# Performance work log

Measured on AMD Instinct MI355X. Metric: run time of the kernel, lower is better.

The kernel has to match this reference:

```python
import jax, jax.numpy as jnp
import numpy as np

B, L, V = 32, 1024, 64
PL = 16                 # patch_len == stride
PH = L // PL            # p_his = 64
PRED = 512
PF = PRED // PL         # p_future = 32
D = 128                 # embed_dim
H = 256                 # hidden_dim
K = 1024                # n_clusters
TOPK = 5
TEMP = 1.0
EPS = 1e-5


def _layernorm(x, w, b):
    mu = jnp.mean(x, axis=-1, keepdims=True)
    var = jnp.mean((x - mu) ** 2, axis=-1, keepdims=True)
    return (x - mu) * jax.lax.rsqrt(var + 1e-5) * w + b


def setup_inputs() -> dict:
    key = jax.random.key(0)
    ks = jax.random.split(key, 12)
    s = 0.02
    return {
        "x": jax.random.normal(ks[0], (B, L, V), jnp.float32),
        "centroids": jax.random.normal(ks[1], (K, D), jnp.float32),
        "enc_w": jax.random.normal(ks[2], (PL, D), jnp.float32) * s,
        "enc_b": jnp.zeros((D,), jnp.float32),
        "ln_w": jnp.ones((D,), jnp.float32),
        "ln_b": jnp.zeros((D,), jnp.float32),
        "fc1_w": jax.random.normal(ks[3], (PH, H), jnp.float32) * s,
        "fc1_b": jnp.zeros((H,), jnp.float32),
        "fcm_w": jax.random.normal(ks[4], (H, 2 * H), jnp.float32) * s,
        "fcm_b": jnp.zeros((2 * H,), jnp.float32),
        "fc2_w": jax.random.normal(ks[5], (2 * H, PF), jnp.float32) * s,
        "fc2_b": jnp.zeros((PF,), jnp.float32),
        "fuse_w": jax.random.normal(ks[6], (D, D), jnp.float32) * s,
        "fuse_b": jnp.zeros((D,), jnp.float32),
        "fln_w": jnp.ones((D,), jnp.float32),
        "fln_b": jnp.zeros((D,), jnp.float32),
        "dec_w": jax.random.normal(ks[7], (D, PL), jnp.float32) * s,
        "dec_b": jnp.zeros((PL,), jnp.float32),
    }


def reference(x, centroids, enc_w, enc_b, ln_w, ln_b, fc1_w, fc1_b, fcm_w, fcm_b,
              fc2_w, fc2_b, fuse_w, fuse_b, fln_w, fln_b, dec_w, dec_b):
    # RevIN 'norm': per-(B,V) instance normalization over L
    mean = jnp.mean(x, axis=1, keepdims=True)               # [B,1,V]
    std = jnp.sqrt(jnp.var(x, axis=1, keepdims=True) + EPS)  # [B,1,V]
    xn = (x - mean) / std
    # patchify: [B,V,L] -> [B,V,PH,PL] (stride == patch_len)
    patches = jnp.transpose(xn, (0, 2, 1)).reshape(B, V, PH, PL)
    # vqvae.encode: per-patch linear patch_len -> D
    z_his = patches @ enc_w + enc_b                          # [B,V,PH,D]
    # TemporalMLPProjector: mix along the patch axis per channel dim
    h = _layernorm(z_his, ln_w, ln_b)
    h = jnp.transpose(h, (0, 1, 3, 2)).reshape(-1, PH)       # [B*V*D, PH]
    h = jax.nn.relu(h @ fc1_w + fc1_b)
    h = jax.nn.relu(h @ fcm_w + fcm_b)
    h = h @ fc2_w + fc2_b                                    # [B*V*D, PF]
    z_p = jnp.transpose(h.reshape(B, V, D, PF), (0, 1, 3, 2))  # [B,V,PF,D]
    # soft VQ: cdist^2 + top-k nearest + softmax-weighted codebook gather
    z_flat = z_p.reshape(-1, D)                              # [N,D], N=B*V*PF
    z2 = jnp.sum(z_flat ** 2, axis=-1, keepdims=True)        # [N,1]
    c2 = jnp.sum(centroids ** 2, axis=-1)                    # [K]
    zc = z_flat @ centroids.T                                # [N,K] GEMM
    dist = z2 + c2[None, :] - 2.0 * zc                       # [N,K]
    logits = (-dist / TEMP).reshape(B, V, PF, K)
    neg_topk, topk_idx = jax.lax.top_k(-dist, TOPK)          # smallest dists
    weights = jax.nn.softmax(neg_topk / TEMP, axis=-1)       # [N,TOPK]
    topk_c = centroids[topk_idx]                             # [N,TOPK,D] gather
    z_code = jnp.einsum('nk,nkd->nd', weights, topk_c).reshape(B, V, PF, D)
    # ResidualFusion: z_code + ReLU(Linear(z_p)), then LayerNorm
    z_fused = _layernorm(z_code + jax.nn.relu(z_p @ fuse_w + fuse_b), fln_w, fln_b)
    # vqvae.decode: per-patch linear D -> patch_len, then unpatchify
    rec_patches = z_fused @ dec_w + dec_b                    # [B,V,PF,PL]
    recon = jnp.transpose(rec_patches.reshape(B, V, PRED), (0, 2, 1))  # [B,PRED,V]
    outputs = recon * std + mean                              # RevIN 'denorm'
    return outputs, logits
```

## Files before the change

### kernel.cpp

```cpp
#include <hip/hip_runtime.h>
#include <float.h>
#include <math.h>


typedef __attribute__((ext_vector_type(8))) short bf16x8;
typedef __attribute__((ext_vector_type(4))) float f32x4;

__device__ __forceinline__ unsigned short f2bf(float f) {
  unsigned int u = __float_as_uint(f);
  u += 0x7FFFu + ((u >> 16) & 1u);
  return (unsigned short)(u >> 16);
}

__global__ __launch_bounds__(1024)
void k_stats(const float* __restrict__ x, float* __restrict__ stats) {
  __shared__ float s1[16][64];
  __shared__ float s2[16][64];
  const int v = threadIdx.x, seg = threadIdx.y, b = blockIdx.x;
  float a = 0.f, aa = 0.f;
  const float* xp = x + (b * 1024 + seg * 64) * 64 + v;
  for (int i = 0; i < 64; ++i) { const float t = xp[i * 64]; a += t; aa += t * t; }
  s1[seg][v] = a; s2[seg][v] = aa;
  __syncthreads();
  if (seg == 0) {
    float S = 0.f, SS = 0.f;
    for (int j = 0; j < 16; ++j) { S += s1[j][v]; SS += s2[j][v]; }
    const float mu  = S * (1.f / 1024.f);
    const float var = SS * (1.f / 1024.f) - mu * mu;
    const float sd  = sqrtf(var + 1e-5f);
    stats[b * 64 + v]        = mu;
    stats[2048 + b * 64 + v] = 1.f / sd;
    stats[4096 + b * 64 + v] = sd;
  }
}

__global__ __launch_bounds__(256)
void k_c2(const float* __restrict__ centroids, float* __restrict__ c2) {
  const int k = blockIdx.x * 256 + threadIdx.x;
  const float* cp = centroids + k * 128;
  float s = 0.f;
  for (int d = 0; d < 128; d += 4) {
    const float4 c = *(const float4*)(cp + d);
    s += c.x * c.x + c.y * c.y + c.z * c.z + c.w * c.w;
  }
  c2[k] = s;
}

__global__ __launch_bounds__(256)
void k_pack(const float* __restrict__ fc1_w, const float* __restrict__ fcm_w,
            const float* __restrict__ fc2_w,
            unsigned short* __restrict__ pk1, unsigned short* __restrict__ pk2,
            unsigned short* __restrict__ pk3) {
  const int idx = blockIdx.x * 256 + threadIdx.x;
  const int l  = idx & 63;
  const int kb = (l >> 4) * 8, nb = l & 15;
  unsigned short t[8];
  if (idx < 2048) {
    const int nt = idx >> 7, ks = (idx >> 6) & 1;
#pragma unroll
    for (int j = 0; j < 8; ++j)
      t[j] = f2bf(fc1_w[(ks * 32 + kb + j) * 256 + nt * 16 + nb]);
#pragma unroll
    for (int j = 0; j < 8; ++j) pk1[idx * 8 + j] = t[j];
  } else if (idx < 18432) {
    const int i2 = idx - 2048;
    const int nt = i2 >> 9, ks = (i2 >> 6) & 7;
#pragma unroll
    for (int j = 0; j < 8; ++j)
      t[j] = f2bf(fcm_w[(ks * 32 + kb + j) * 512 + nt * 16 + nb]);
#pragma unroll
    for (int j = 0; j < 8; ++j) pk2[i2 * 8 + j] = t[j];
  } else {
    const int i3 = idx - 18432;
    const int nt = i3 >> 10, ks = (i3 >> 6) & 15;
#pragma unroll
    for (int j = 0; j < 8; ++j)
      t[j] = f2bf(fc2_w[(ks * 32 + kb + j) * 32 + nt * 16 + nb]);
#pragma unroll
    for (int j = 0; j < 8; ++j) pk3[i3 * 8 + j] = t[j];
  }
}

__global__ __launch_bounds__(256)
void k_pack2(const float* __restrict__ centroids, const float* __restrict__ fuse_w,
             unsigned short* __restrict__ pkc, unsigned short* __restrict__ pkf) {
  const int idx = blockIdx.x * 256 + threadIdx.x;
  const int l  = idx & 63;
  const int kb = (l >> 4) * 8, nb = l & 15;
  unsigned short t[8];
  if (idx < 16384) {
    const int nt = idx >> 8;
#pragma unroll
    for (int j = 0; j < 8; ++j)
      t[j] = f2bf(centroids[(nt * 16 + nb) * 128 + ((idx >> 6) & 3) * 32 + kb + j]);
#pragma unroll
    for (int j = 0; j < 8; ++j) pkc[idx * 8 + j] = t[j];
  } else {
    const int i2 = idx - 16384;
    const int nt = i2 >> 8, ks = (i2 >> 6) & 3;
#pragma unroll
    for (int j = 0; j < 8; ++j)
      t[j] = f2bf(fuse_w[(ks * 32 + kb + j) * 128 + nt * 16 + nb]);
#pragma unroll
    for (int j = 0; j < 8; ++j) pkf[i2 * 8 + j] = t[j];
  }
}

__global__ __launch_bounds__(256, 2)
void k_mlp(const float* __restrict__ x,
           const float* __restrict__ enc_w, const float* __restrict__ enc_b,
           const float* __restrict__ ln_w,  const float* __restrict__ ln_b,
           const float* __restrict__ fc1_b, const float* __restrict__ fcm_b,
           const float* __restrict__ fc2_b,
           const unsigned short* __restrict__ pk1,
           const unsigned short* __restrict__ pk2,
           const unsigned short* __restrict__ pk3,
           const float* __restrict__ stats, float* __restrict__ z_p) {
  __shared__ __align__(16) char smem[65536];
  unsigned short* sh0 = (unsigned short*)smem;
  unsigned short* sh1 = (unsigned short*)(smem + 16384);
  unsigned short* sh2 = (unsigned short*)(smem + 49152);
  float* sxn = (float*)(smem + 16384);
  float* red = (float*)(smem + 20480);
  float* sew = (float*)(smem + 49152);

  const int tid  = threadIdx.x;
  const int lane = tid & 63, wv = tid >> 6;
  const int l15  = lane & 15, l16 = lane >> 4;
  const int bv   = blockIdx.x, b = bv >> 6, v = bv & 63;

  {
    const float mn = stats[bv], rs = stats[2048 + bv];
    const float* xb = x + b * 65536 + v;
    for (int i = tid; i < 1024; i += 256) sxn[i] = (xb[i * 64] - mn) * rs;
    for (int i = tid; i < 2048; i += 256) sew[i] = enc_w[i];
    __syncthreads();
    const int p = tid >> 2, qd = tid & 3;
    float xr[16];
#pragma unroll
    for (int t = 0; t < 16; ++t) xr[t] = sxn[p * 16 + t];
    float zv[32];
    float s1 = 0.f, s2 = 0.f;
#pragma unroll
    for (int dl = 0; dl < 32; ++dl) {
      const int d = qd * 32 + dl;
      float z = enc_b[d];
#pragma unroll
      for (int t = 0; t < 16; ++t) z += xr[t] * sew[t * 128 + d];
      zv[dl] = z; s1 += z; s2 += z * z;
    }
    red[p * 4 + qd] = s1; red[256 + p * 4 + qd] = s2;
    __syncthreads();
    const float S1 = red[p * 4] + red[p * 4 + 1] + red[p * 4 + 2] + red[p * 4 + 3];
    const float S2 = red[256 + p * 4] + red[256 + p * 4 + 1] +
                     red[256 + p * 4 + 2] + red[256 + p * 4 + 3];
    const float mu  = S1 * (1.f / 128.f);
    const float rsd = rsqrtf(S2 * (1.f / 128.f) - mu * mu + 1e-5f);
#pragma unroll
    for (int dl = 0; dl < 32; ++dl) {
      const int d = qd * 32 + dl;
      const float zn = (zv[dl] - mu) * rsd * ln_w[d] + ln_b[d];
      sh0[(d * 64 + p) ^ ((d & 7) << 3)] = f2bf(zn);
    }
  }
  __syncthreads();

  for (int hf = 0; hf < 2; ++hf) {
    {
      bf16x8 bf1[4][2];
#pragma unroll
      for (int nt = 0; nt < 4; ++nt) {
        const int ntg = wv * 4 + nt;
#pragma unroll
        for (int ks = 0; ks < 2; ++ks)
          bf1[nt][ks] = *(const bf16x8*)(pk1 + (((ntg * 2 + ks) * 64 + lane) << 3));
      }
      const int swa = (l15 & 7) << 3;
      bf16x8 am[4][2];
#pragma unroll
      for (int m = 0; m < 4; ++m) {
        const int row = hf * 64 + m * 16 + l15;
#pragma unroll
        for (int ks = 0; ks < 2; ++ks)
          am[m][ks] = *(const bf16x8*)(sh0 + ((row * 64 + ks * 32 + l16 * 8) ^ swa));
      }
      f32x4 acc1[4][4];
#pragma unroll
      for (int nt = 0; nt < 4; ++nt)
#pragma unroll
        for (int m = 0; m < 4; ++m) {
          f32x4 a; a[0] = 0.f; a[1] = 0.f; a[2] = 0.f; a[3] = 0.f;
          a = __builtin_amdgcn_mfma_f32_16x16x32_bf16(am[m][0], bf1[nt][0], a, 0, 0, 0);
          a = __builtin_amdgcn_mfma_f32_16x16x32_bf16(am[m][1], bf1[nt][1], a, 0, 0, 0);
          acc1[nt][m] = a;
        }
#pragma unroll
      for (int nt = 0; nt < 4; ++nt) {
        const int n = (wv * 4 + nt) * 16 + l15;
        const float bb = fc1_b[n];
#pragma unroll
        for (int m = 0; m < 4; ++m)
#pragma unroll
          for (int j = 0; j < 4; ++j) {
            const int r = m * 16 + l16 * 4 + j;
            const float vv = acc1[nt][m][j] + bb;
            sh1[(r * 256 + n) ^ ((r & 7) << 3)] = f2bf(vv > 0.f ? vv : 0.f);
          }
      }
    }
    __syncthreads();

    f32x4 accz[2];
#pragma unroll
    for (int nt = 0; nt < 2; ++nt) {
      const float bz = fc2_b[nt * 16 + l15];
      accz[nt][0] = bz; accz[nt][1] = bz; accz[nt][2] = bz; accz[nt][3] = bz;
    }

    for (int it = 0; it < 4; ++it) {
      bf16x8 bf2[2][8];
#pragma unroll
      for (int nt = 0; nt < 2; ++nt) {
        const int ntg = it * 8 + wv * 2 + nt;
#pragma unroll
        for (int ks = 0; ks < 8; ++ks)
          bf2[nt][ks] = *(const bf16x8*)(pk2 + (((ntg * 8 + ks) * 64 + lane) << 3));
      }
      f32x4 acc2[2][4];
#pragma unroll
      for (int nt = 0; nt < 2; ++nt)
#pragma unroll
        for (int m = 0; m < 4; ++m) {
          acc2[nt][m][0] = 0.f; acc2[nt][m][1] = 0.f;
          acc2[nt][m][2] = 0.f; acc2[nt][m][3] = 0.f;
        }
#pragma unroll
      for (int ks = 0; ks < 8; ++ks) {
        bf16x8 a2[4];
#pragma unroll
        for (int m = 0; m < 4; ++m) {
          const int row = m * 16 + l15;
          a2[m] = *(const bf16x8*)(sh1 +
                    ((row * 256 + ks * 32 + l16 * 8) ^ ((row & 7) << 3)));
        }
#pragma unroll
        for (int nt = 0; nt < 2; ++nt)
#pragma unroll
          for (int m = 0; m < 4; ++m)
            acc2[nt][m] = __builtin_amdgcn_mfma_f32_16x16x32_bf16(
                a2[m], bf2[nt][ks], acc2[nt][m], 0, 0, 0);
      }
#pragma unroll
      for (int nt = 0; nt < 2; ++nt) {
        const float bb = fcm_b[(it * 8 + wv * 2 + nt) * 16 + l15];
        const int c = (wv * 2 + nt) * 16 + l15;
#pragma unroll
        for (int m = 0; m < 4; ++m)
#pragma unroll
          for (int j = 0; j < 4; ++j) {
            const int r = m * 16 + l16 * 4 + j;
            const float vv = acc2[nt][m][j] + bb;
            sh2[(r * 128 + c) ^ ((r & 7) << 3)] = f2bf(vv > 0.f ? vv : 0.f);
          }
      }
      __syncthreads();
      {
        const int row = wv * 16 + l15;
        const int sw  = (row & 7) << 3;
        bf16x8 b3[2][4];
#pragma unroll
        for (int nt = 0; nt < 2; ++nt)
#pragma unroll
          for (int ks = 0; ks < 4; ++ks)
            b3[nt][ks] = *(const bf16x8*)(pk3 +
                           (((nt * 16 + it * 4 + ks) * 64 + lane) << 3));
#pragma unroll
        for (int ks = 0; ks < 4; ++ks) {
          const bf16x8 a3 = *(const bf16x8*)(sh2 +
                              ((row * 128 + ks * 32 + l16 * 8) ^ sw));
#pragma unroll
          for (int nt = 0; nt < 2; ++nt)
            accz[nt] = __builtin_amdgcn_mfma_f32_16x16x32_bf16(
                a3, b3[nt][ks], accz[nt], 0, 0, 0);
        }
      }
      __syncthreads();
    }

    {
      const int d0 = hf * 64 + wv * 16 + l16 * 4;
#pragma unroll
      for (int nt = 0; nt < 2; ++nt) {
        const int f = nt * 16 + l15;
        *(float4*)(z_p + (bv * 32 + f) * 128 + d0) =
            make_float4(accz[nt][0], accz[nt][1], accz[nt][2], accz[nt][3]);
      }
    }
  }
}

__global__ __launch_bounds__(256)
void k_vq(const float* __restrict__ z_p, const float* __restrict__ centroids,
          const float* __restrict__ c2g,
          const unsigned short* __restrict__ pkc,
          const unsigned short* __restrict__ pkf,
          const float* __restrict__ fuse_b,
          const float* __restrict__ fln_w,  const float* __restrict__ fln_b,
          const float* __restrict__ dec_w,  const float* __restrict__ dec_b,
          const float* __restrict__ stats,
          float* __restrict__ outputs, float* __restrict__ logits) {
  __shared__ __align__(16) char smem[23680];
  float* sdist = (float*)smem;
  float* zc    = (float*)smem;
  unsigned int* cand = (unsigned int*)(smem + 16896);
  float* z2s    = (float*)(smem + 22016);
  float* wrow   = (float*)(smem + 22144);
  int*   irow   = (int*)  (smem + 22784);
  float* lnstat = (float*)(smem + 23424);

  const int tid  = threadIdx.x;
  const int lane = tid & 63, wv = tid >> 6;
  const int l15  = lane & 15, l16 = lane >> 4;
  const int bv   = blockIdx.x, b = bv >> 6, v = bv & 63;

  bf16x8 za[2][4];
#pragma unroll
  for (int m = 0; m < 2; ++m)
#pragma unroll
    for (int ks = 0; ks < 4; ++ks) {
      const float* zp = z_p + (bv * 32 + m * 16 + l15) * 128 + ks * 32 + l16 * 8;
      const float4 u0 = *(const float4*)zp;
      const float4 u1 = *(const float4*)(zp + 4);
      bf16x8 t;
      t[0] = (short)f2bf(u0.x); t[1] = (short)f2bf(u0.y);
      t[2] = (short)f2bf(u0.z); t[3] = (short)f2bf(u0.w);
      t[4] = (short)f2bf(u1.x); t[5] = (short)f2bf(u1.y);
      t[6] = (short)f2bf(u1.z); t[7] = (short)f2bf(u1.w);
      za[m][ks] = t;
    }

  if (tid < 32) {
    const float* zp = z_p + (bv * 32 + tid) * 128;
    float s = 0.f;
    for (int d = 0; d < 128; d += 4) {
      const float4 u = *(const float4*)(zp + d);
      s += u.x * u.x + u.y * u.y + u.z * u.z + u.w * u.w;
    }
    z2s[tid] = s;
  }
  __syncthreads();

  float z2r[2][4];
#pragma unroll
  for (int m = 0; m < 2; ++m)
#pragma unroll
    for (int j = 0; j < 4; ++j) z2r[m][j] = z2s[m * 16 + l16 * 4 + j];

  unsigned int d5[5];
#pragma unroll
  for (int s = 0; s < 5; ++s) d5[s] = 0xFFFFFFFFu;

  const int row8 = tid >> 3, strip = tid & 7;

  for (int cc = 0; cc < 8; ++cc) {
    bf16x8 bfc[2][4];
#pragma unroll
    for (int nt = 0; nt < 2; ++nt) {
      const int ntg = cc * 8 + wv * 2 + nt;
#pragma unroll
      for (int ks = 0; ks < 4; ++ks)
        bfc[nt][ks] = *(const bf16x8*)(pkc + (((ntg * 4 + ks) * 64 + lane) << 3));
    }
    f32x4 acc[2][2];
#pragma unroll
    for (int nt = 0; nt < 2; ++nt)
#pragma unroll
      for (int m = 0; m < 2; ++m) {
        f32x4 a; a[0] = 0.f; a[1] = 0.f; a[2] = 0.f; a[3] = 0.f;
#pragma unroll
        for (int ks = 0; ks < 4; ++ks)
          a = __builtin_amdgcn_mfma_f32_16x16x32_bf16(za[m][ks], bfc[nt][ks], a, 0, 0, 0);
        acc[nt][m] = a;
      }
    if (cc) __syncthreads();
    {
      const float c2a = c2g[cc * 128 + (wv * 2) * 16 + l15];
      const float c2b = c2g[cc * 128 + (wv * 2 + 1) * 16 + l15];
#pragma unroll
      for (int nt = 0; nt < 2; ++nt) {
        const int colc = (wv * 2 + nt) * 16 + l15;
        const float cc2 = nt ? c2b : c2a;
#pragma unroll
        for (int m = 0; m < 2; ++m)
#pragma unroll
          for (int j = 0; j < 4; ++j) {
            const int r = m * 16 + l16 * 4 + j;
            sdist[r * 132 + colc] = z2r[m][j] + cc2 - 2.f * acc[nt][m][j];
          }
      }
    }
    __syncthreads();
#pragma unroll
    for (int i = 0; i < 4; ++i) {
      const int row = i * 8 + wv * 2 + (lane >> 5);
      const int c4  = (lane & 31) * 4;
      const float4 dv = *(const float4*)(sdist + row * 132 + c4);
      *(float4*)(logits + (bv * 32 + row) * 1024 + cc * 128 + c4) =
          make_float4(-dv.x, -dv.y, -dv.z, -dv.w);
    }
    for (int c = 0; c < 16; ++c) {
      const int col = strip + 8 * c;
      const float dvv = sdist[row8 * 132 + col];
      const unsigned int key =
          (__float_as_uint(dvv) & 0xFFFFFC00u) | (unsigned)(cc * 128 + col);
      if (key < d5[4]) {
        d5[4] = key;
        unsigned int t;
        if (d5[4] < d5[3]) { t = d5[3]; d5[3] = d5[4]; d5[4] = t; }
        if (d5[3] < d5[2]) { t = d5[2]; d5[2] = d5[3]; d5[3] = t; }
        if (d5[2] < d5[1]) { t = d5[1]; d5[1] = d5[2]; d5[2] = t; }
        if (d5[1] < d5[0]) { t = d5[0]; d5[0] = d5[1]; d5[1] = t; }
      }
    }
  }

#pragma unroll
  for (int s = 0; s < 5; ++s) cand[row8 * 40 + strip * 5 + s] = d5[s];
  __syncthreads();
  if (tid < 32) {
    unsigned int bk[5];
    for (int s = 0; s < 5; ++s) {
      unsigned int best = 0xFFFFFFFFu; int bpos = 0;
      for (int c = 0; c < 40; ++c) {
        const unsigned int u = cand[tid * 40 + c];
        if (u < best) { best = u; bpos = c; }
      }
      bk[s] = best; cand[tid * 40 + bpos] = 0xFFFFFFFFu;
    }
    float df[5];
#pragma unroll
    for (int j = 0; j < 5; ++j) df[j] = __uint_as_float(bk[j] & 0xFFFFFC00u);
    float e[5]; float sum = 0.f;
#pragma unroll
    for (int j = 0; j < 5; ++j) { e[j] = expf(df[0] - df[j]); sum += e[j]; }
    const float inv = 1.f / sum;
#pragma unroll
    for (int j = 0; j < 5; ++j) {
      wrow[tid * 5 + j] = e[j] * inv;
      irow[tid * 5 + j] = (int)(bk[j] & 1023u);
    }
  }
  __syncthreads();

  {
    const int r = tid >> 3, d0 = (tid & 7) * 16;
    float acc[16];
#pragma unroll
    for (int dd = 0; dd < 16; ++dd) acc[dd] = 0.f;
    for (int j = 0; j < 5; ++j) {
      const float w = wrow[r * 5 + j];
      const int   k = irow[r * 5 + j];
      const float* cp = centroids + k * 128 + d0;
#pragma unroll
      for (int dd = 0; dd < 16; dd += 4) {
        const float4 cv = *(const float4*)(cp + dd);
        acc[dd]   += w * cv.x; acc[dd+1] += w * cv.y;
        acc[dd+2] += w * cv.z; acc[dd+3] += w * cv.w;
      }
    }
#pragma unroll
    for (int dd = 0; dd < 16; dd += 4)
      *(float4*)(zc + r * 132 + d0 + dd) =
          make_float4(acc[dd], acc[dd+1], acc[dd+2], acc[dd+3]);
  }

  f32x4 fac[2][2];
  {
    bf16x8 bff[2][4];
#pragma unroll
    for (int nt = 0; nt < 2; ++nt) {
      const int ntg = wv * 2 + nt;
#pragma unroll
      for (int ks = 0; ks < 4; ++ks)
        bff[nt][ks] = *(const bf16x8*)(pkf + (((ntg * 4 + ks) * 64 + lane) << 3));
    }
#pragma unroll
    for (int nt = 0; nt < 2; ++nt)
#pragma unroll
      for (int m = 0; m < 2; ++m) {
        f32x4 a; a[0] = 0.f; a[1] = 0.f; a[2] = 0.f; a[3] = 0.f;
#pragma unroll
        for (int ks = 0; ks < 4; ++ks)
          a = __builtin_amdgcn_mfma_f32_16x16x32_bf16(za[m][ks], bff[nt][ks], a, 0, 0, 0);
        fac[nt][m] = a;
      }
  }
  __syncthreads();
#pragma unroll
  for (int nt = 0; nt < 2; ++nt) {
    const int colc = (wv * 2 + nt) * 16 + l15;
    const float fbv = fuse_b[colc];
#pragma unroll
    for (int m = 0; m < 2; ++m)
#pragma unroll
      for (int j = 0; j < 4; ++j) {
        const int r = m * 16 + l16 * 4 + j;
        zc[r * 132 + colc] += fmaxf(fac[nt][m][j] + fbv, 0.f);
      }
  }
  __syncthreads();

  if (tid < 32) {
    float s = 0.f, ss = 0.f;
    for (int d = 0; d < 128; ++d) { const float t = zc[tid * 132 + d]; s += t; ss += t * t; }
    const float mu  = s * (1.f / 128.f);
    const float var = ss * (1.f / 128.f) - mu * mu;
    lnstat[tid * 2]     = mu;
    lnstat[tid * 2 + 1] = rsqrtf(var + 1e-5f);
  }
  __syncthreads();

  {
    const int r = tid >> 3, tt = (tid & 7) * 2;
    const float mu = lnstat[r * 2], rsd = lnstat[r * 2 + 1];
    float o0 = dec_b[tt], o1 = dec_b[tt + 1];
    for (int d = 0; d < 128; ++d) {
      const float zf = (zc[r * 132 + d] - mu) * rsd * fln_w[d] + fln_b[d];
      o0 += zf * dec_w[d * 16 + tt];
      o1 += zf * dec_w[d * 16 + tt + 1];
    }
    const float sd = stats[4096 + bv], mn = stats[bv];
    outputs[(b * 512 + r * 16 + tt) * 64 + v]     = o0 * sd + mn;
    outputs[(b * 512 + r * 16 + tt + 1) * 64 + v] = o1 * sd + mn;
  }
}

extern "C" void kernel_launch(void* const* d_in, const int* in_sizes, int n_in,
                              void* d_out, int out_size, void* d_ws, size_t ws_size,
                              hipStream_t stream) {
  const float* x      = (const float*)d_in[0];
  const float* cent   = (const float*)d_in[1];
  const float* enc_w  = (const float*)d_in[2];
  const float* enc_b  = (const float*)d_in[3];
  const float* ln_w   = (const float*)d_in[4];
  const float* ln_b   = (const float*)d_in[5];
  const float* fc1_w  = (const float*)d_in[6];
  const float* fc1_b  = (const float*)d_in[7];
  const float* fcm_w  = (const float*)d_in[8];
  const float* fcm_b  = (const float*)d_in[9];
  const float* fc2_w  = (const float*)d_in[10];
  const float* fc2_b  = (const float*)d_in[11];
  const float* fuse_w = (const float*)d_in[12];
  const float* fuse_b = (const float*)d_in[13];
  const float* fln_w  = (const float*)d_in[14];
  const float* fln_b  = (const float*)d_in[15];
  const float* dec_w  = (const float*)d_in[16];
  const float* dec_b  = (const float*)d_in[17];

  float* ws    = (float*)d_ws;
  float* stats = ws;
  float* c2    = ws + 6144;
  float* z_p   = ws + 8192;
  unsigned short* pku = (unsigned short*)(ws + 8192 + 65536 * 128);
  unsigned short* pk1 = pku;
  unsigned short* pk2 = pku + 16384;
  unsigned short* pk3 = pku + 147456;
  unsigned short* pkc = pku + 163840;
  unsigned short* pkf = pku + 294912;

  float* outputs = (float*)d_out;
  float* logits  = (float*)d_out + 32 * 512 * 64;

  k_stats<<<dim3(32), dim3(64, 16), 0, stream>>>(x, stats);
  k_c2<<<dim3(4), dim3(256), 0, stream>>>(cent, c2);
  k_pack<<<dim3(80), dim3(256), 0, stream>>>(fc1_w, fcm_w, fc2_w, pk1, pk2, pk3);
  k_pack2<<<dim3(72), dim3(256), 0, stream>>>(cent, fuse_w, pkc, pkf);
  k_mlp<<<dim3(2048), dim3(256), 0, stream>>>(x, enc_w, enc_b, ln_w, ln_b,
      fc1_b, fcm_b, fc2_b, pk1, pk2, pk3, stats, z_p);
  k_vq<<<dim3(2048), dim3(256), 0, stream>>>(z_p, cent, c2, pkc, pkf, fuse_b,
      fln_w, fln_b, dec_w, dec_b, stats, outputs, logits);
}
```

Baseline: 600.4 us.

## Split fc2 reduction across waves by K-slice and drop per-iteration barriers

Each wave now multiplies only its own slice of the fc2 reduction dimension, using the sh2 columns it wrote itself, over all four row tiles. This removes the two __syncthreads per fcm/fc2 iteration. The partial sums from the four waves go to shared memory and are reduced, biased and stored to z_p in a final pass. The cost is more accumulator registers, an extra shared-memory staging and reduction step, and a smaller swizzle on sh2 writes that may bring back bank conflicts.

Result: slower. 637.3 us (+6.2%).

```diff
diff --git a/kernel.cpp b/kernel.cpp
--- a/kernel.cpp
+++ b/kernel.cpp
@@ -210,12 +210,14 @@
     }
     __syncthreads();
 
-    f32x4 accz[2];
-#pragma unroll
-    for (int nt = 0; nt < 2; ++nt) {
-      const float bz = fc2_b[nt * 16 + l15];
-      accz[nt][0] = bz; accz[nt][1] = bz; accz[nt][2] = bz; accz[nt][3] = bz;
-    }
+    f32x4 accz[2][4];
+#pragma unroll
+    for (int nt = 0; nt < 2; ++nt)
+#pragma unroll
+      for (int m = 0; m < 4; ++m) {
+        accz[nt][m][0] = 0.f; accz[nt][m][1] = 0.f;
+        accz[nt][m][2] = 0.f; accz[nt][m][3] = 0.f;
+      }
 
     for (int it = 0; it < 4; ++it) {
       bf16x8 bf2[2][8];
@@ -260,42 +262,57 @@
           for (int j = 0; j < 4; ++j) {
             const int r = m * 16 + l16 * 4 + j;
             const float vv = acc2[nt][m][j] + bb;
-            sh2[(r * 128 + c) ^ ((r & 7) << 3)] = f2bf(vv > 0.f ? vv : 0.f);
+            sh2[(r * 128 + c) ^ ((r & 3) << 3)] = f2bf(vv > 0.f ? vv : 0.f);
           }
       }
-      __syncthreads();
       {
-        const int row = wv * 16 + l15;
-        const int sw  = (row & 7) << 3;
-        bf16x8 b3[2][4];
+        bf16x8 b3[2];
 #pragma unroll
         for (int nt = 0; nt < 2; ++nt)
-#pragma unroll
-          for (int ks = 0; ks < 4; ++ks)
-            b3[nt][ks] = *(const bf16x8*)(pk3 +
-                           (((nt * 16 + it * 4 + ks) * 64 + lane) << 3));
-#pragma unroll
-        for (int ks = 0; ks < 4; ++ks) {
+          b3[nt] = *(const bf16x8*)(pk3 +
+                     (((nt * 16 + it * 4 + wv) * 64 + lane) << 3));
+#pragma unroll
+        for (int mt = 0; mt < 4; ++mt) {
+          const int row = mt * 16 + l15;
           const bf16x8 a3 = *(const bf16x8*)(sh2 +
-                              ((row * 128 + ks * 32 + l16 * 8) ^ sw));
+                              ((row * 128 + wv * 32 + l16 * 8) ^ ((row & 3) << 3)));
 #pragma unroll
           for (int nt = 0; nt < 2; ++nt)
-            accz[nt] = __builtin_amdgcn_mfma_f32_16x16x32_bf16(
-                a3, b3[nt][ks], accz[nt], 0, 0, 0);
+            accz[nt][mt] = __builtin_amdgcn_mfma_f32_16x16x32_bf16(
+                a3, b3[nt], accz[nt][mt], 0, 0, 0);
         }
       }
-      __syncthreads();
-    }
+    }
+    __syncthreads();
 
     {
-      const int d0 = hf * 64 + wv * 16 + l16 * 4;
+      float* part = (float*)(smem + 16384) + wv * 3072;
 #pragma unroll
       for (int nt = 0; nt < 2; ++nt) {
         const int f = nt * 16 + l15;
-        *(float4*)(z_p + (bv * 32 + f) * 128 + d0) =
-            make_float4(accz[nt][0], accz[nt][1], accz[nt][2], accz[nt][3]);
-      }
-    }
+#pragma unroll
+        for (int m = 0; m < 4; ++m)
+#pragma unroll
+          for (int j = 0; j < 4; ++j)
+            part[(m * 16 + l16 * 4 + j) * 33 + f] = accz[nt][m][j];
+      }
+    }
+    __syncthreads();
+    {
+      const float* P = (float*)(smem + 16384);
+      const int f = tid >> 3, r0 = (tid & 7) * 8;
+      const float bz = fc2_b[f];
+      float o[8];
+#pragma unroll
+      for (int e = 0; e < 8; ++e) {
+        const int i = (r0 + e) * 33 + f;
+        o[e] = P[i] + P[3072 + i] + P[6144 + i] + P[9216 + i] + bz;
+      }
+      float* zp = z_p + (bv * 32 + f) * 128 + hf * 64 + r0;
+      *(float4*)(zp)     = make_float4(o[0], o[1], o[2], o[3]);
+      *(float4*)(zp + 4) = make_float4(o[4], o[5], o[6], o[7]);
+    }
+    __syncthreads();
   }
 }
 
```
